# Kernel optimization log

Measured on AMD Instinct MI355X. Metric: run time of the kernel, lower is better.

Reference implementation:

```python
import jax, jax.numpy as jnp
import numpy as np
import math, itertools


def _dct_consts():
    t = np.zeros((8, 8, 8, 8), dtype=np.float32)
    for x, y, u, v in itertools.product(range(8), repeat=4):
        t[x, y, u, v] = math.cos((2 * x + 1) * u * math.pi / 16) * math.cos((2 * y + 1) * v * math.pi / 16)
    alpha = np.array([1.0 / np.sqrt(2)] + [1.0] * 7, dtype=np.float32)
    scale = np.outer(alpha, alpha).astype(np.float32) * 0.25
    return jnp.asarray(t), jnp.asarray(scale)

_TENSOR, _SCALE = _dct_consts()


def setup_inputs() -> dict:
    key = jax.random.key(0)
    # 64 RGB 512x512 images unfolded into 8x8 blocks: [B, C, n_blocks, 8, 8]
    image = jax.random.uniform(key, (64, 3, 4096, 8, 8), dtype=jnp.float32) * 255.0
    return {"image": image}


def reference(image) -> jnp.ndarray:
    x = image - 128.0
    # tensordot(image, tensor, dims=2): contract last two spatial dims (x,y)
    # with basis -> frequency dims (u,v); then elementwise scale.
    out = _SCALE * jnp.einsum('...xy,xyuv->...uv', x, _TENSOR)
    return out.reshape(image.shape)
```

## Files before the change

kernel.cpp:

```cpp
#include <hip/hip_runtime.h>

typedef float fx4 __attribute__((ext_vector_type(4)));

__device__ __forceinline__ void dct8(const float a[8], float o[8]) {
    const float s0 = a[0] + a[7], s1 = a[1] + a[6], s2 = a[2] + a[5], s3 = a[3] + a[4];
    const float d0 = a[0] - a[7], d1 = a[1] - a[6], d2 = a[2] - a[5], d3 = a[3] - a[4];
    const float ss0 = s0 + s3, ss1 = s1 + s2;
    const float ds0 = s0 - s3, ds1 = s1 - s2;
    o[0] = ss0 + ss1;
    o[4] = 0.70710678f * (ss0 - ss1);
    o[2] = fmaf(0.92387953f, ds0,  0.38268343f * ds1);
    o[6] = fmaf(0.38268343f, ds0, -0.92387953f * ds1);
    o[1] = fmaf(0.98078528f, d0, fmaf( 0.83146961f, d1, fmaf( 0.55557023f, d2,  0.19509032f * d3)));
    o[3] = fmaf(0.83146961f, d0, fmaf(-0.19509032f, d1, fmaf(-0.98078528f, d2, -0.55557023f * d3)));
    o[5] = fmaf(0.55557023f, d0, fmaf(-0.98078528f, d1, fmaf( 0.19509032f, d2,  0.83146961f * d3)));
    o[7] = fmaf(0.19509032f, d0, fmaf(-0.55557023f, d1, fmaf( 0.83146961f, d2, -0.98078528f * d3)));
}

__global__ __launch_bounds__(256) void dct8x8_kernel(const float* __restrict__ in,
                                                     float* __restrict__ out) {
    __shared__ alignas(16) float lds1[32 * 68];

    const int tid  = blockIdx.x * 256 + threadIdx.x;
    const int l    = threadIdx.x & 7;
    const int base = (threadIdx.x >> 3) * 68;
    const int cbase = base + (l & 4) * 8 + (l & 3);

    const fx4* p = reinterpret_cast<const fx4*>(in) + (size_t)tid * 2;
    fx4 v0 = __builtin_nontemporal_load(p);
    fx4 v1 = __builtin_nontemporal_load(p + 1);
    float a[8] = { v0[0], v0[1], v0[2], v0[3], v1[0], v1[1], v1[2], v1[3] };

    float r[8];
    dct8(a, r);
    r[0] -= 1024.0f;

    fx4 w0 = { r[0], r[1], r[2], r[3] };
    fx4 w1 = { r[4], r[5], r[6], r[7] };
    *reinterpret_cast<fx4*>(&lds1[base + l * 4])      = w0;
    *reinterpret_cast<fx4*>(&lds1[base + 32 + l * 4]) = w1;

    float t[8];
#pragma unroll
    for (int y = 0; y < 8; ++y) t[y] = lds1[cbase + y * 4];

    float o[8];
    dct8(t, o);

    const float sl = (l == 0) ? 0.35355339059f : 0.5f;
#pragma unroll
    for (int u = 0; u < 8; ++u) o[u] *= sl * ((u == 0) ? 0.35355339059f : 0.5f);

#pragma unroll
    for (int u = 0; u < 8; ++u) lds1[cbase + u * 4] = o[u];

    fx4 q0 = *reinterpret_cast<const fx4*>(&lds1[base + l * 4]);
    fx4 q1 = *reinterpret_cast<const fx4*>(&lds1[base + 32 + l * 4]);

    fx4* qp = reinterpret_cast<fx4*>(out) + (size_t)tid * 2;
    qp[0] = q0;
    qp[1] = q1;
}

extern "C" void kernel_launch(void* const* d_in, const int* in_sizes, int n_in,
                              void* d_out, int out_size, void* d_ws, size_t ws_size,
                              hipStream_t stream) {
    const float* in = (const float*)d_in[0];
    float* out = (float*)d_out;
    const int n = in_sizes[0];
    const int nthreads = n / 8;
    const int grid = (nthreads + 255) / 256;
    hipLaunchKernelGGL(dct8x8_kernel, dim3(grid), dim3(256), 0, stream,
                       in, out);
}
```

Baseline: 75.87 us.

## Use persistent grid-stride loop with register prefetch of next row

Replaces the one-row-per-thread launch with a fixed grid of 2048 blocks that loop over rows in grid-stride fashion. Each iteration issues the nontemporal loads for the next row before doing the current row's DCT and LDS transpose, so memory latency overlaps compute. The aim is to cut block launch overhead and hide load latency, at the cost of fewer waves in flight and extra registers. niter is computed by integer division and nrows goes unused, so any remainder rows would be dropped unless the row count divides evenly.

Result: slower. 82.90 us (+9.3%).

```diff
diff --git a/kernel.cpp b/kernel.cpp
--- a/kernel.cpp
+++ b/kernel.cpp
@@ -18,48 +18,65 @@
 }
 
 __global__ __launch_bounds__(256) void dct8x8_kernel(const float* __restrict__ in,
-                                                     float* __restrict__ out) {
+                                                     float* __restrict__ out,
+                                                     int nrows, int niter) {
     __shared__ alignas(16) float lds1[32 * 68];
 
-    const int tid  = blockIdx.x * 256 + threadIdx.x;
-    const int l    = threadIdx.x & 7;
-    const int base = (threadIdx.x >> 3) * 68;
+    const int l     = threadIdx.x & 7;
+    const int base  = (threadIdx.x >> 3) * 68;
     const int cbase = base + (l & 4) * 8 + (l & 3);
+    const int gstride = gridDim.x * 256;
 
-    const fx4* p = reinterpret_cast<const fx4*>(in) + (size_t)tid * 2;
-    fx4 v0 = __builtin_nontemporal_load(p);
-    fx4 v1 = __builtin_nontemporal_load(p + 1);
-    float a[8] = { v0[0], v0[1], v0[2], v0[3], v1[0], v1[1], v1[2], v1[3] };
+    const fx4* __restrict__ p = reinterpret_cast<const fx4*>(in);
+    fx4* __restrict__ q = reinterpret_cast<fx4*>(out);
 
-    float r[8];
-    dct8(a, r);
-    r[0] -= 1024.0f;
+    size_t idx = (size_t)blockIdx.x * 256 + threadIdx.x;
 
-    fx4 w0 = { r[0], r[1], r[2], r[3] };
-    fx4 w1 = { r[4], r[5], r[6], r[7] };
-    *reinterpret_cast<fx4*>(&lds1[base + l * 4])      = w0;
-    *reinterpret_cast<fx4*>(&lds1[base + 32 + l * 4]) = w1;
+    fx4 v0 = __builtin_nontemporal_load(p + idx * 2);
+    fx4 v1 = __builtin_nontemporal_load(p + idx * 2 + 1);
 
-    float t[8];
+    for (int it = 0; it < niter; ++it) {
+        const size_t nidx = idx + gstride;
+        fx4 n0, n1;
+        if (it + 1 < niter) {
+            n0 = __builtin_nontemporal_load(p + nidx * 2);
+            n1 = __builtin_nontemporal_load(p + nidx * 2 + 1);
+        }
+
+        float a[8] = { v0[0], v0[1], v0[2], v0[3], v1[0], v1[1], v1[2], v1[3] };
+        float r[8];
+        dct8(a, r);
+        r[0] -= 1024.0f;
+
+        fx4 w0 = { r[0], r[1], r[2], r[3] };
+        fx4 w1 = { r[4], r[5], r[6], r[7] };
+        *reinterpret_cast<fx4*>(&lds1[base + l * 4])      = w0;
+        *reinterpret_cast<fx4*>(&lds1[base + 32 + l * 4]) = w1;
+
+        float t[8];
 #pragma unroll
-    for (int y = 0; y < 8; ++y) t[y] = lds1[cbase + y * 4];
+        for (int y = 0; y < 8; ++y) t[y] = lds1[cbase + y * 4];
 
-    float o[8];
-    dct8(t, o);
+        float o[8];
+        dct8(t, o);
 
-    const float sl = (l == 0) ? 0.35355339059f : 0.5f;
+        const float sl = (l == 0) ? 0.35355339059f : 0.5f;
 #pragma unroll
-    for (int u = 0; u < 8; ++u) o[u] *= sl * ((u == 0) ? 0.35355339059f : 0.5f);
+        for (int u = 0; u < 8; ++u) o[u] *= sl * ((u == 0) ? 0.35355339059f : 0.5f);
 
 #pragma unroll
-    for (int u = 0; u < 8; ++u) lds1[cbase + u * 4] = o[u];
+        for (int u = 0; u < 8; ++u) lds1[cbase + u * 4] = o[u];
 
-    fx4 q0 = *reinterpret_cast<const fx4*>(&lds1[base + l * 4]);
-    fx4 q1 = *reinterpret_cast<const fx4*>(&lds1[base + 32 + l * 4]);
+        fx4 q0 = *reinterpret_cast<const fx4*>(&lds1[base + l * 4]);
+        fx4 q1 = *reinterpret_cast<const fx4*>(&lds1[base + 32 + l * 4]);
 
-    fx4* qp = reinterpret_cast<fx4*>(out) + (size_t)tid * 2;
-    qp[0] = q0;
-    qp[1] = q1;
+        q[idx * 2]     = q0;
+        q[idx * 2 + 1] = q1;
+
+        idx = nidx;
+        v0 = n0;
+        v1 = n1;
+    }
 }
 
 extern "C" void kernel_launch(void* const* d_in, const int* in_sizes, int n_in,
@@ -68,8 +85,9 @@
     const float* in = (const float*)d_in[0];
     float* out = (float*)d_out;
     const int n = in_sizes[0];
-    const int nthreads = n / 8;
-    const int grid = (nthreads + 255) / 256;
+    const int nrows = n / 8;
+    const int grid = 2048;
+    const int niter = nrows / (grid * 256);
     hipLaunchKernelGGL(dct8x8_kernel, dim3(grid), dim3(256), 0, stream,
-                       in, out);
+                       in, out, nrows, niter);
 }
```
